# Kernel optimization log

Measured on AMD Instinct MI355X. Metric: run time of the kernel, lower is better.

The kernel has to match this reference:

```python
import jax, jax.numpy as jnp
import numpy as np

N, E, G = 50000, 800000, 1024
F_IN, GH, HEADS, MH = 128, 64, 4, 64
C1 = GH // 2  # 32 per-head channels in gat1


def _p(key, shape, scale=0.05):
    return (scale * jax.random.normal(key, shape)).astype(jnp.float32)


def setup_inputs() -> dict:
    key = jax.random.key(0)
    ks = jax.random.split(key, 24)
    x = jax.random.normal(ks[0], (N, F_IN), dtype=jnp.float32)
    edge_index = jax.random.randint(ks[1], (2, E), 0, N, dtype=jnp.int64)
    batch = jnp.sort(jax.random.randint(ks[2], (N,), 0, G, dtype=jnp.int64))
    return {
        "x": x, "edge_index": edge_index, "batch": batch,
        # node_proj
        "Wp": _p(ks[3], (F_IN, GH)), "bp": jnp.zeros((GH,), jnp.float32),
        # gat1: in GH, out C1 per head, 4 heads, concat
        "W1": _p(ks[4], (GH, HEADS * C1)), "as1": _p(ks[5], (HEADS, C1)),
        "ad1": _p(ks[6], (HEADS, C1)), "b1": jnp.zeros((HEADS * C1,), jnp.float32),
        # gat2: in HEADS*C1=128, out GH, 1 head, no concat
        "W2": _p(ks[7], (HEADS * C1, GH)), "as2": _p(ks[8], (1, GH)),
        "ad2": _p(ks[9], (1, GH)), "b2": jnp.zeros((GH,), jnp.float32),
        # mlp + heads
        "Wm1": _p(ks[10], (GH, MH)), "bm1": jnp.zeros((MH,), jnp.float32),
        "Wm2": _p(ks[11], (MH, MH)), "bm2": jnp.zeros((MH,), jnp.float32),
        "Wc": _p(ks[12], (MH, 1)), "bc": jnp.zeros((1,), jnp.float32),
        "Wr": _p(ks[13], (MH, 1)), "br": jnp.zeros((1,), jnp.float32),
        "Wv": _p(ks[14], (MH, 1)), "bv": jnp.zeros((1,), jnp.float32),
    }


def gat_conv(h, src, dst, W, att_src, att_dst, bias, heads, out_ch, concat):
    n = h.shape[0]
    xh = (h @ W).reshape(n, heads, out_ch)          # [N,H,C]
    a_s = jnp.einsum("nhc,hc->nh", xh, att_src)      # [N,H]
    a_d = jnp.einsum("nhc,hc->nh", xh, att_dst)
    e = jax.nn.leaky_relu(a_s[src] + a_d[dst], 0.2)  # [E,H]
    # segment softmax over incoming edges of each dst node
    m = jax.ops.segment_max(e, dst, num_segments=n)
    e = jnp.exp(e - m[dst])
    denom = jax.ops.segment_sum(e, dst, num_segments=n)
    alpha = e / (denom[dst] + 1e-16)                 # [E,H]
    msg = xh[src] * alpha[:, :, None]                # [E,H,C]
    out = jax.ops.segment_sum(msg, dst, num_segments=n)
    out = out.reshape(n, heads * out_ch) if concat else out.mean(axis=1)
    return out + bias


def reference(x, edge_index, batch, Wp, bp, W1, as1, ad1, b1, W2, as2, ad2, b2,
              Wm1, bm1, Wm2, bm2, Wc, bc, Wr, br, Wv, bv):
    n = x.shape[0]
    loops = jnp.arange(n, dtype=edge_index.dtype)
    src = jnp.concatenate([edge_index[0], loops])  # PyG add_self_loops=True
    dst = jnp.concatenate([edge_index[1], loops])

    h = jax.nn.relu(x @ Wp + bp)
    h = jax.nn.elu(gat_conv(h, src, dst, W1, as1, ad1, b1, HEADS, C1, True))
    h = jax.nn.elu(gat_conv(h, src, dst, W2, as2, ad2, b2, 1, GH, False))

    # global mean pool over graphs
    sums = jax.ops.segment_sum(h, batch, num_segments=G)
    cnts = jax.ops.segment_sum(jnp.ones((n,), h.dtype), batch, num_segments=G)
    hg = sums / jnp.maximum(cnts, 1.0)[:, None]      # [G, GH]

    z = jax.nn.relu(hg @ Wm1 + bm1)
    z = jax.nn.relu(z @ Wm2 + bm2)
    class_logit = (z @ Wc + bc)[:, 0]
    ret = (z @ Wr + br)[:, 0]
    vol = jax.nn.softplus((z @ Wv + bv)[:, 0])
    return class_logit, ret, vol
```

## Files before the change

kernel.cpp:

```cpp
#include <hip/hip_runtime.h>
#include <hip/hip_bf16.h>
#include <math.h>

#define F_IN 128
#define GH   64

typedef __attribute__((ext_vector_type(8))) short bf16x8;
typedef __attribute__((ext_vector_type(4))) float f32x4;

__device__ __forceinline__ void edge_sd(const int* __restrict__ ei, int E, int e, int& s, int& d) {
    if (e < E) { s = ei[e]; d = ei[E + e]; } else { s = d = e - E; }
}
__device__ __forceinline__ float leaky(float x) { return (x >= 0.f) ? x : 0.2f * x; }
__device__ __forceinline__ unsigned short f2bf(float f) {
    unsigned u = __float_as_uint(f);
    u += 0x7FFFu + ((u >> 16) & 1u);
    return (unsigned short)(u >> 16);
}
__device__ __forceinline__ float bflo(unsigned v) { return __uint_as_float(v << 16); }
__device__ __forceinline__ float bfhi(unsigned v) { return __uint_as_float(v & 0xFFFF0000u); }

template<int K, int M, bool RELU, int AIN, int DOTS>
__global__ __launch_bounds__(256) void gemm_mfma(
    const float* __restrict__ Xf, const unsigned short* __restrict__ Xb,
    const float* __restrict__ W, const float* __restrict__ Bias,
    unsigned short* __restrict__ Yb,
    const float* __restrict__ asw, const float* __restrict__ adw,
    float* __restrict__ as_n, float* __restrict__ ad_n, int nrows)
{
    constexpr int KP = K + 8;
    __shared__ unsigned short Als[64 * KP];
    __shared__ unsigned short Wls[M * KP];
    const int t = threadIdx.x;
    const int base = blockIdx.x * 64;

    for (int i = t; i < K * M / 4; i += 256) {
        int k  = i / (M / 4);
        int m0 = (i % (M / 4)) * 4;
        float4 wv = ((const float4*)W)[i];
        Wls[(m0 + 0) * KP + k] = f2bf(wv.x);
        Wls[(m0 + 1) * KP + k] = f2bf(wv.y);
        Wls[(m0 + 2) * KP + k] = f2bf(wv.z);
        Wls[(m0 + 3) * KP + k] = f2bf(wv.w);
    }
    if (AIN == 0) {
        for (int i = t; i < 64 * K / 4; i += 256) {
            int r  = i / (K / 4);
            int c4 = (i % (K / 4)) * 4;
            int n = base + r;
            float4 v = make_float4(0.f, 0.f, 0.f, 0.f);
            if (n < nrows) v = ((const float4*)(Xf + (size_t)n * K))[c4 >> 2];
            ushort4 pk = make_ushort4(f2bf(v.x), f2bf(v.y), f2bf(v.z), f2bf(v.w));
            *(ushort4*)&Als[r * KP + c4] = pk;
        }
    } else {
        for (int i = t; i < 64 * K / 8; i += 256) {
            int r  = i / (K / 8);
            int c8 = (i % (K / 8)) * 8;
            int n = base + r;
            uint4 v = make_uint4(0, 0, 0, 0);
            if (n < nrows) v = ((const uint4*)(Xb + (size_t)n * K))[c8 >> 3];
            *(uint4*)&Als[r * KP + c8] = v;
        }
    }
    __syncthreads();

    const int w = t >> 6, l = t & 63;
    const int lr = l & 15, lg = l >> 4;
    constexpr int CT = M / 16;
    f32x4 acc[CT];
#pragma unroll
    for (int ct = 0; ct < CT; ct++) acc[ct] = (f32x4){0.f, 0.f, 0.f, 0.f};

    const unsigned short* arow = &Als[(w * 16 + lr) * KP + lg * 8];
#pragma unroll
    for (int ks = 0; ks < K / 32; ks++) {
        bf16x8 a = *(const bf16x8*)(arow + ks * 32);
#pragma unroll
        for (int ct = 0; ct < CT; ct++) {
            bf16x8 b = *(const bf16x8*)&Wls[(ct * 16 + lr) * KP + ks * 32 + lg * 8];
            acc[ct] = __builtin_amdgcn_mfma_f32_16x16x32_bf16(a, b, acc[ct], 0, 0, 0);
        }
    }

#pragma unroll
    for (int ct = 0; ct < CT; ct++) {
        int col = ct * 16 + lr;
        float bb = Bias ? Bias[col] : 0.f;
#pragma unroll
        for (int r = 0; r < 4; r++) {
            int gr = base + w * 16 + lg * 4 + r;
            if (gr < nrows) {
                float v = acc[ct][r] + bb;
                if (RELU) v = fmaxf(v, 0.f);
                Yb[(size_t)gr * M + col] = f2bf(v);
            }
        }
    }

    if (DOTS == 1) {
        float hs[4][4], hd[4][4];
#pragma unroll
        for (int r = 0; r < 4; r++)
#pragma unroll
            for (int h = 0; h < 4; h++) { hs[r][h] = 0.f; hd[r][h] = 0.f; }
#pragma unroll
        for (int ct = 0; ct < CT; ct++) {
            int col = ct * 16 + lr;
            float aw = asw[col], dw = adw[col];
            int h = ct >> 1;
#pragma unroll
            for (int r = 0; r < 4; r++) {
                hs[r][h] += acc[ct][r] * aw;
                hd[r][h] += acc[ct][r] * dw;
            }
        }
#pragma unroll
        for (int msk = 8; msk >= 1; msk >>= 1) {
#pragma unroll
            for (int r = 0; r < 4; r++)
#pragma unroll
                for (int h = 0; h < 4; h++) {
                    hs[r][h] += __shfl_xor(hs[r][h], msk);
                    hd[r][h] += __shfl_xor(hd[r][h], msk);
                }
        }
        if (lr == 0) {
#pragma unroll
            for (int r = 0; r < 4; r++) {
                int gr = base + w * 16 + lg * 4 + r;
                if (gr < nrows) {
                    ((float4*)as_n)[gr] = make_float4(hs[r][0], hs[r][1], hs[r][2], hs[r][3]);
                    ((float4*)ad_n)[gr] = make_float4(hd[r][0], hd[r][1], hd[r][2], hd[r][3]);
                }
            }
        }
    } else if (DOTS == 2) {
        float ps[4], pd[4];
#pragma unroll
        for (int r = 0; r < 4; r++) { ps[r] = 0.f; pd[r] = 0.f; }
#pragma unroll
        for (int ct = 0; ct < CT; ct++) {
            int col = ct * 16 + lr;
            float aw = asw[col], dw = adw[col];
#pragma unroll
            for (int r = 0; r < 4; r++) {
                ps[r] += acc[ct][r] * aw;
                pd[r] += acc[ct][r] * dw;
            }
        }
#pragma unroll
        for (int msk = 8; msk >= 1; msk >>= 1) {
#pragma unroll
            for (int r = 0; r < 4; r++) {
                ps[r] += __shfl_xor(ps[r], msk);
                pd[r] += __shfl_xor(pd[r], msk);
            }
        }
        if (lr == 0) {
#pragma unroll
            for (int r = 0; r < 4; r++) {
                int gr = base + w * 16 + lg * 4 + r;
                if (gr < nrows) { as_n[gr] = ps[r]; ad_n[gr] = pd[r]; }
            }
        }
    }
}

__global__ __launch_bounds__(256) void bucket_hist(
    const int* __restrict__ ei, int E, int ET, int N, int* __restrict__ bcnt)
{
    __shared__ int h[256];
    h[threadIdx.x] = 0;
    __syncthreads();
    for (int e = blockIdx.x * 256 + threadIdx.x; e < ET; e += gridDim.x * 256) {
        int s, d; edge_sd(ei, E, e, s, d);
        if ((unsigned)s < (unsigned)N && (unsigned)d < (unsigned)N)
            atomicAdd(&h[d >> 8], 1);
    }
    __syncthreads();
    if (h[threadIdx.x]) atomicAdd(&bcnt[threadIdx.x], h[threadIdx.x]);
}

__global__ __launch_bounds__(256) void bucket_scan(
    const int* __restrict__ bcnt, int* __restrict__ bbase, int* __restrict__ bcur,
    int* __restrict__ row_start, int B, int N)
{
    __shared__ int wsum[4];
    int t = threadIdx.x, lane = t & 63, w = t >> 6;
    int v = (t < B) ? bcnt[t] : 0;
    int incl = v;
#pragma unroll
    for (int off = 1; off < 64; off <<= 1) {
        int n = __shfl_up(incl, off);
        if (lane >= off) incl += n;
    }
    if (lane == 63) wsum[w] = incl;
    __syncthreads();
    int wb = 0;
#pragma unroll
    for (int i = 0; i < 4; i++) if (i < w) wb += wsum[i];
    int excl = wb + incl - v;
    if (t < B) { bbase[t] = excl; bcur[t] = excl; }
    if (t == 255) { bbase[B] = excl + v; row_start[N] = excl + v; }
}

#define SCHUNK 4096
__global__ __launch_bounds__(256) void bucket_scatter(
    const int* __restrict__ ei, int E, int ET, int N,
    int* __restrict__ bcur, int* __restrict__ deg, uint2* __restrict__ staged)
{
    __shared__ int bc[256];
    __shared__ int bb[256];
    const int t = threadIdx.x;
    const int base = blockIdx.x * SCHUNK;
    bc[t] = 0;
    __syncthreads();
    const int cnt = min(SCHUNK, ET - base);
    int ss[16], dd[16], lr[16];
#pragma unroll
    for (int k = 0; k < 16; k++) {
        int i = t + k * 256;
        ss[k] = -1; dd[k] = 0; lr[k] = 0;
        if (i < cnt) {
            int s, d; edge_sd(ei, E, base + i, s, d);
            if ((unsigned)s < (unsigned)N && (unsigned)d < (unsigned)N) {
                ss[k] = s; dd[k] = d;
                lr[k] = atomicAdd(&bc[d >> 8], 1);
                atomicAdd(&deg[d], 1);
            }
        }
    }
    __syncthreads();
    bb[t] = bc[t] ? atomicAdd(&bcur[t], bc[t]) : 0;
    __syncthreads();
#pragma unroll
    for (int k = 0; k < 16; k++) {
        if (ss[k] >= 0)
            staged[bb[dd[k] >> 8] + lr[k]] = make_uint2((unsigned)ss[k], (unsigned)dd[k]);
    }
}

__global__ __launch_bounds__(256) void row_scan(
    const int* __restrict__ deg, const int* __restrict__ bbase,
    int* __restrict__ row_start, int N)
{
    __shared__ int wsum[4];
    const int b = blockIdx.x, t = threadIdx.x;
    const int lane = t & 63, w = t >> 6;
    const int node = b * 256 + t;
    int v = (node < N) ? deg[node] : 0;
    int incl = v;
#pragma unroll
    for (int off = 1; off < 64; off <<= 1) {
        int n = __shfl_up(incl, off);
        if (lane >= off) incl += n;
    }
    if (lane == 63) wsum[w] = incl;
    __syncthreads();
    int wb = 0;
#pragma unroll
    for (int i = 0; i < 4; i++) if (i < w) wb += wsum[i];
    if (node < N) row_start[node] = bbase[b] + wb + incl - v;
}

__global__ __launch_bounds__(256) void bucket_final(
    const uint2* __restrict__ staged, const int* __restrict__ bbase,
    const int* __restrict__ row_start, int* __restrict__ adj, int N)
{
    __shared__ int cur[256];
    const int b = blockIdx.x, t = threadIdx.x;
    const int node = b * 256 + t;
    cur[t] = (node < N) ? row_start[node] : 0;
    __syncthreads();
    const int beg = bbase[b], end = bbase[b + 1];
    for (int i = beg + t; i < end; i += 256) {
        uint2 sd = staged[i];
        int pos = atomicAdd(&cur[sd.y & 255], 1);
        adj[pos] = (int)sd.x;
    }
}

__global__ __launch_bounds__(256) void gat1_fused(
    const int* __restrict__ row_start, const int* __restrict__ adj,
    const float* __restrict__ as_n, const float* __restrict__ ad_n,
    const unsigned short* __restrict__ xhb, const float* __restrict__ b1,
    unsigned short* __restrict__ outb, int N)
{
    __shared__ unsigned s_ofs[4][64];
    __shared__ float    s_p[4][256];
    const int w = threadIdx.x >> 6;
    const int d = blockIdx.x * 4 + w;
    if (d >= N) return;
    const int lane = threadIdx.x & 63;
    const int li = lane & 31;
    const int half = lane >> 5;
    const int h = li >> 3;
    const int beg = row_start[d];
    const int deg = row_start[d + 1] - beg;
    const float4 adv = ((const float4*)ad_n)[d];
    const char* xbase = (const char*)xhb;

    float l0 = 0.f, l1 = 0.f, l2 = 0.f, l3 = 0.f;
    float a0 = 0.f, a1 = 0.f, a2 = 0.f, a3 = 0.f;
    for (int j0 = 0; j0 < deg; j0 += 64) {
        const int chunk = min(64, deg - j0);
        if (lane < chunk) {
            int s = adj[beg + j0 + lane];
            float4 asv = ((const float4*)as_n)[s];
            float p0 = __expf(leaky(asv.x + adv.x));
            float p1 = __expf(leaky(asv.y + adv.y));
            float p2 = __expf(leaky(asv.z + adv.z));
            float p3 = __expf(leaky(asv.w + adv.w));
            l0 += p0; l1 += p1; l2 += p2; l3 += p3;
            s_ofs[w][lane] = (unsigned)s << 8;
            ((float4*)&s_p[w][lane * 4])[0] = make_float4(p0, p1, p2, p3);
        }
        __threadfence_block();
#pragma unroll 4
        for (int jj = half; jj < chunk; jj += 2) {
            float a = s_p[w][jj * 4 + h];
            unsigned ofs = s_ofs[w][jj] + ((unsigned)li << 3);
            uint2 u = *(const uint2*)(xbase + ofs);
            a0 += a * bflo(u.x); a1 += a * bfhi(u.x);
            a2 += a * bflo(u.y); a3 += a * bfhi(u.y);
        }
        __threadfence_block();
    }
    a0 += __shfl_xor(a0, 32); a1 += __shfl_xor(a1, 32);
    a2 += __shfl_xor(a2, 32); a3 += __shfl_xor(a3, 32);
#pragma unroll
    for (int msk = 32; msk >= 1; msk >>= 1) {
        l0 += __shfl_xor(l0, msk); l1 += __shfl_xor(l1, msk);
        l2 += __shfl_xor(l2, msk); l3 += __shfl_xor(l3, msk);
    }
    if (half == 0) {
        float lh = (h == 0) ? l0 : (h == 1) ? l1 : (h == 2) ? l2 : l3;
        const float inv = 1.0f / (lh + 1e-16f);
        float4 bb = ((const float4*)b1)[li];
        float v0 = a0 * inv + bb.x;
        float v1 = a1 * inv + bb.y;
        float v2 = a2 * inv + bb.z;
        float v3 = a3 * inv + bb.w;
        v0 = (v0 > 0.f) ? v0 : expm1f(v0);
        v1 = (v1 > 0.f) ? v1 : expm1f(v1);
        v2 = (v2 > 0.f) ? v2 : expm1f(v2);
        v3 = (v3 > 0.f) ? v3 : expm1f(v3);
        unsigned pk01 = (unsigned)f2bf(v0) | ((unsigned)f2bf(v1) << 16);
        unsigned pk23 = (unsigned)f2bf(v2) | ((unsigned)f2bf(v3) << 16);
        ((uint2*)((char*)outb + (size_t)d * 256))[li] = make_uint2(pk01, pk23);
    }
}

__global__ __launch_bounds__(256) void gat2_fused(
    const int* __restrict__ row_start, const int* __restrict__ adj,
    const float* __restrict__ as_n, const float* __restrict__ ad_n,
    const unsigned short* __restrict__ xhb, const float* __restrict__ b2,
    const int* __restrict__ batch, float* __restrict__ sums, float* __restrict__ cnts,
    int N, int G)
{
    __shared__ unsigned s_ofs[4][64];
    __shared__ float    s_p[4][64];
    __shared__ float    pbuf[4][64];
    __shared__ int      pg[4];
    const int w = threadIdx.x >> 6;
    const int d = blockIdx.x * 4 + w;
    const int lane = threadIdx.x & 63;
    const int li = lane & 31;
    const int half = lane >> 5;
    const bool alive = (d < N);
    int beg = 0, deg = 0; float ad = 0.f; int g = -1;
    if (alive) {
        beg = row_start[d];
        deg = row_start[d + 1] - beg;
        ad = ad_n[d];
        int gb = batch[d];
        if ((unsigned)gb < (unsigned)G) g = gb;
    }
    const char* xbase = (const char*)xhb;
    float l = 0.f, a0 = 0.f, a1 = 0.f;
    for (int j0 = 0; j0 < deg; j0 += 64) {
        const int chunk = min(64, deg - j0);
        if (lane < chunk) {
            int s = adj[beg + j0 + lane];
            float p = __expf(leaky(as_n[s] + ad));
            l += p;
            s_ofs[w][lane] = (unsigned)s << 7;
            s_p[w][lane] = p;
        }
        __threadfence_block();
#pragma unroll 4
        for (int jj = half; jj < chunk; jj += 2) {
            float a = s_p[w][jj];
            unsigned ofs = s_ofs[w][jj] + ((unsigned)li << 2);
            unsigned u = *(const unsigned*)(xbase + ofs);
            a0 += a * bflo(u);
            a1 += a * bfhi(u);
        }
        __threadfence_block();
    }
    a0 += __shfl_xor(a0, 32);
    a1 += __shfl_xor(a1, 32);
#pragma unroll
    for (int msk = 32; msk >= 1; msk >>= 1) l += __shfl_xor(l, msk);

    if (lane == 0) pg[w] = g;
    if (half == 0) {
        const float inv = 1.0f / (l + 1e-16f);
        float2 bb = ((const float2*)b2)[li];
        float v0 = a0 * inv + bb.x;
        float v1 = a1 * inv + bb.y;
        v0 = (v0 > 0.f) ? v0 : expm1f(v0);
        v1 = (v1 > 0.f) ? v1 : expm1f(v1);
        ((float2*)&pbuf[w][2 * li])[0] = make_float2((g >= 0) ? v0 : 0.f,
                                                    (g >= 0) ? v1 : 0.f);
    }
    __syncthreads();
    int g0 = pg[0], g1 = pg[1], g2 = pg[2], g3 = pg[3];
    bool uni = (g0 >= 0) && (g1 == g0) && (g2 == g0) && (g3 == g0);
    if (uni) {
        if (w == 0) {
            float s4 = pbuf[0][lane] + pbuf[1][lane] + pbuf[2][lane] + pbuf[3][lane];
            atomicAdd(&sums[(size_t)g0 * 64 + lane], s4);
            if (lane == 0) atomicAdd(&cnts[g0], 4.0f);
        }
    } else if (g >= 0) {
        atomicAdd(&sums[(size_t)g * 64 + lane], pbuf[w][lane]);
        if (lane == 0) atomicAdd(&cnts[g], 1.0f);
    }
}

__global__ __launch_bounds__(64) void mlp_head(
    const float* __restrict__ sums, const float* __restrict__ cnts,
    const float* __restrict__ Wm1, const float* __restrict__ bm1,
    const float* __restrict__ Wm2, const float* __restrict__ bm2,
    const float* __restrict__ Wc, const float* __restrict__ bc,
    const float* __restrict__ Wr, const float* __restrict__ br,
    const float* __restrict__ Wv, const float* __restrict__ bv,
    float* __restrict__ out, int G)
{
    int g = blockIdx.x;
    int t = threadIdx.x;
    __shared__ float hrow[64];
    __shared__ float zrow[64];
    float hv = sums[(size_t)g * 64 + t] / fmaxf(cnts[g], 1.0f);
    hrow[t] = hv;
    __syncthreads();
    float z1 = bm1[t];
#pragma unroll 8
    for (int k = 0; k < 64; k++) z1 += hrow[k] * Wm1[k * 64 + t];
    z1 = fmaxf(z1, 0.f);
    zrow[t] = z1;
    __syncthreads();
    float z2 = bm2[t];
#pragma unroll 8
    for (int k = 0; k < 64; k++) z2 += zrow[k] * Wm2[k * 64 + t];
    z2 = fmaxf(z2, 0.f);
    float pc = z2 * Wc[t], pr = z2 * Wr[t], pv = z2 * Wv[t];
#pragma unroll
    for (int m = 32; m >= 1; m >>= 1) {
        pc += __shfl_xor(pc, m);
        pr += __shfl_xor(pr, m);
        pv += __shfl_xor(pv, m);
    }
    if (t == 0) {
        out[g] = pc + bc[0];
        out[G + g] = pr + br[0];
        float s = pv + bv[0];
        out[2 * G + g] = (s > 20.f) ? s : log1pf(expf(s));
    }
}

extern "C" void kernel_launch(void* const* d_in, const int* in_sizes, int n_in,
                              void* d_out, int out_size, void* d_ws, size_t ws_size,
                              hipStream_t stream)
{
    const float* x     = (const float*)d_in[0];
    const int*   ei    = (const int*)d_in[1];
    const int*   batch = (const int*)d_in[2];
    const float* Wp  = (const float*)d_in[3];
    const float* bp  = (const float*)d_in[4];
    const float* W1  = (const float*)d_in[5];
    const float* as1 = (const float*)d_in[6];
    const float* ad1 = (const float*)d_in[7];
    const float* b1  = (const float*)d_in[8];
    const float* W2  = (const float*)d_in[9];
    const float* as2 = (const float*)d_in[10];
    const float* ad2 = (const float*)d_in[11];
    const float* b2  = (const float*)d_in[12];
    const float* Wm1 = (const float*)d_in[13];
    const float* bm1 = (const float*)d_in[14];
    const float* Wm2 = (const float*)d_in[15];
    const float* bm2 = (const float*)d_in[16];
    const float* Wc  = (const float*)d_in[17];
    const float* bc  = (const float*)d_in[18];
    const float* Wr  = (const float*)d_in[19];
    const float* br  = (const float*)d_in[20];
    const float* Wv  = (const float*)d_in[21];
    const float* bv  = (const float*)d_in[22];

    const int N  = in_sizes[0] / F_IN;
    const int E  = in_sizes[1] / 2;
    const int G  = out_size / 3;
    const int ET = E + N;
    const int B  = (N + 255) >> 8;

    float* ws = (float*)d_ws;
    size_t o = 0;
    unsigned short* h0b  = (unsigned short*)(ws + o); o += (size_t)N * 32;
    unsigned short* h1b  = (unsigned short*)(ws + o); o += (size_t)N * 64;
    unsigned short* xhb1 = (unsigned short*)(ws + o); o += (size_t)N * 64;
    unsigned short* xhb2 = (unsigned short*)(ws + o); o += (size_t)N * 32;
    float* as1n = ws + o; o += (size_t)N * 4;
    float* ad1n = ws + o; o += (size_t)N * 4;
    float* as2n = ws + o; o += (size_t)N;
    float* ad2n = ws + o; o += (size_t)N;
    int* row_start = (int*)(ws + o); o += (size_t)N + 1;
    int* adj       = (int*)(ws + o); o += (size_t)ET;
    int* bbase     = (int*)(ws + o); o += 257;
    int* bcur      = (int*)(ws + o); o += 256;
    uint2* staged  = (uint2*)(ws + o); o += (size_t)ET * 2;
    float* zstart = ws + o;
    int*   deg  = (int*)(ws + o); o += (size_t)N;
    int*   bcnt = (int*)(ws + o); o += 256;
    float* sums = ws + o;         o += (size_t)G * 64;
    float* cnts = ws + o;         o += (size_t)G;
    size_t zlen = (size_t)(ws + o - zstart) * sizeof(float);

    hipMemsetAsync(zstart, 0, zlen, stream);

    const int gN64 = (N + 63) / 64;
    const int gN4  = (N + 3) / 4;
    const int gSC  = (ET + SCHUNK - 1) / SCHUNK;

    bucket_hist<<<512, 256, 0, stream>>>(ei, E, ET, N, bcnt);
    bucket_scan<<<1, 256, 0, stream>>>(bcnt, bbase, bcur, row_start, B, N);
    bucket_scatter<<<gSC, 256, 0, stream>>>(ei, E, ET, N, bcur, deg, staged);
    row_scan<<<B, 256, 0, stream>>>(deg, bbase, row_start, N);
    bucket_final<<<B, 256, 0, stream>>>(staged, bbase, row_start, adj, N);

    gemm_mfma<128, 64, true, 0, 0><<<gN64, 256, 0, stream>>>(
        x, nullptr, Wp, bp, h0b, nullptr, nullptr, nullptr, nullptr, N);
    gemm_mfma<64, 128, false, 1, 1><<<gN64, 256, 0, stream>>>(
        nullptr, h0b, W1, nullptr, xhb1, as1, ad1, as1n, ad1n, N);
    gat1_fused<<<gN4, 256, 0, stream>>>(row_start, adj, as1n, ad1n, xhb1, b1, h1b, N);
    gemm_mfma<128, 64, false, 1, 2><<<gN64, 256, 0, stream>>>(
        nullptr, h1b, W2, nullptr, xhb2, as2, ad2, as2n, ad2n, N);
    gat2_fused<<<gN4, 256, 0, stream>>>(row_start, adj, as2n, ad2n, xhb2, b2,
                                        batch, sums, cnts, N, G);
    mlp_head<<<G, 64, 0, stream>>>(sums, cnts, Wm1, bm1, Wm2, bm2,
                                   Wc, bc, Wr, br, Wv, bv, (float*)d_out, G);
}
```

Measured before the change: 321.2 us.

## Locally sort edges in LDS and pack staged entries to cut CSR build traffic

The bucket scatter now counts per-bucket edges in shared memory, sorts each chunk's edges by bucket in LDS, and writes them to the staging buffer as contiguous runs. Each edge is packed into one 32-bit word (bucket, low dst bits, src), replacing the 8-byte pair. The global per-node degree atomics and the separate row_scan kernel are gone: a new bucket_build kernel counts degrees per bucket in LDS, scans them to write row_start, and fills adj. This aims to remove global atomic contention, scattered staging writes and one launch, at the cost of reading the edge list twice and limiting node ids to 16 bits (N < 65536).

After: 293.6 us. 8.6% less time.

```diff
diff --git a/kernel.cpp b/kernel.cpp
--- a/kernel.cpp
+++ b/kernel.cpp
@@ -205,79 +205,99 @@
     if (t == 255) { bbase[B] = excl + v; row_start[N] = excl + v; }
 }
 
-#define SCHUNK 4096
+#define SCHUNK 2048
 __global__ __launch_bounds__(256) void bucket_scatter(
     const int* __restrict__ ei, int E, int ET, int N,
-    int* __restrict__ bcur, int* __restrict__ deg, uint2* __restrict__ staged)
+    int* __restrict__ bcur, unsigned* __restrict__ staged)
 {
     __shared__ int bc[256];
+    __shared__ int lbase[256];
     __shared__ int bb[256];
+    __shared__ unsigned sorted[SCHUNK];
+    __shared__ int wsum[4];
     const int t = threadIdx.x;
+    const int lane = t & 63, wv = t >> 6;
     const int base = blockIdx.x * SCHUNK;
+    const int cnt = min(SCHUNK, ET - base);
     bc[t] = 0;
     __syncthreads();
-    const int cnt = min(SCHUNK, ET - base);
-    int ss[16], dd[16], lr[16];
-#pragma unroll
-    for (int k = 0; k < 16; k++) {
-        int i = t + k * 256;
-        ss[k] = -1; dd[k] = 0; lr[k] = 0;
-        if (i < cnt) {
-            int s, d; edge_sd(ei, E, base + i, s, d);
-            if ((unsigned)s < (unsigned)N && (unsigned)d < (unsigned)N) {
-                ss[k] = s; dd[k] = d;
-                lr[k] = atomicAdd(&bc[d >> 8], 1);
-                atomicAdd(&deg[d], 1);
-            }
-        }
-    }
-    __syncthreads();
-    bb[t] = bc[t] ? atomicAdd(&bcur[t], bc[t]) : 0;
-    __syncthreads();
-#pragma unroll
-    for (int k = 0; k < 16; k++) {
-        if (ss[k] >= 0)
-            staged[bb[dd[k] >> 8] + lr[k]] = make_uint2((unsigned)ss[k], (unsigned)dd[k]);
-    }
-}
-
-__global__ __launch_bounds__(256) void row_scan(
-    const int* __restrict__ deg, const int* __restrict__ bbase,
-    int* __restrict__ row_start, int N)
-{
-    __shared__ int wsum[4];
-    const int b = blockIdx.x, t = threadIdx.x;
-    const int lane = t & 63, w = t >> 6;
-    const int node = b * 256 + t;
-    int v = (node < N) ? deg[node] : 0;
+    for (int i = t; i < cnt; i += 256) {
+        int s, d; edge_sd(ei, E, base + i, s, d);
+        if ((unsigned)s < (unsigned)N && (unsigned)d < (unsigned)N)
+            atomicAdd(&bc[d >> 8], 1);
+    }
+    __syncthreads();
+    int v = bc[t];
     int incl = v;
 #pragma unroll
     for (int off = 1; off < 64; off <<= 1) {
         int n = __shfl_up(incl, off);
         if (lane >= off) incl += n;
     }
-    if (lane == 63) wsum[w] = incl;
+    if (lane == 63) wsum[wv] = incl;
     __syncthreads();
     int wb = 0;
 #pragma unroll
-    for (int i = 0; i < 4; i++) if (i < w) wb += wsum[i];
-    if (node < N) row_start[node] = bbase[b] + wb + incl - v;
-}
-
-__global__ __launch_bounds__(256) void bucket_final(
-    const uint2* __restrict__ staged, const int* __restrict__ bbase,
-    const int* __restrict__ row_start, int* __restrict__ adj, int N)
-{
-    __shared__ int cur[256];
+    for (int i = 0; i < 4; i++) if (i < wv) wb += wsum[i];
+    int excl = wb + incl - v;
+    lbase[t] = excl;
+    bb[t] = v ? atomicAdd(&bcur[t], v) : 0;
+    __syncthreads();
+    bc[t] = excl;
+    __syncthreads();
+    for (int i = t; i < cnt; i += 256) {
+        int s, d; edge_sd(ei, E, base + i, s, d);
+        if ((unsigned)s < (unsigned)N && (unsigned)d < (unsigned)N) {
+            int b = d >> 8;
+            int r = atomicAdd(&bc[b], 1);
+            sorted[r] = ((unsigned)b << 24) | ((unsigned)(d & 255) << 16) | (unsigned)s;
+        }
+    }
+    __syncthreads();
+    const int total = bc[255];
+    for (int i = t; i < total; i += 256) {
+        unsigned wd = sorted[i];
+        int b = wd >> 24;
+        staged[bb[b] + (i - lbase[b])] = wd;
+    }
+}
+
+__global__ __launch_bounds__(256) void bucket_build(
+    const unsigned* __restrict__ staged, const int* __restrict__ bbase,
+    int* __restrict__ row_start, int* __restrict__ adj, int N)
+{
+    __shared__ int cnt2[256];
+    __shared__ int cur2[256];
+    __shared__ int wsum[4];
     const int b = blockIdx.x, t = threadIdx.x;
-    const int node = b * 256 + t;
-    cur[t] = (node < N) ? row_start[node] : 0;
-    __syncthreads();
+    const int lane = t & 63, wv = t >> 6;
     const int beg = bbase[b], end = bbase[b + 1];
+    cnt2[t] = 0;
+    __syncthreads();
+    for (int i = beg + t; i < end; i += 256)
+        atomicAdd(&cnt2[(staged[i] >> 16) & 255], 1);
+    __syncthreads();
+    int v = cnt2[t];
+    int incl = v;
+#pragma unroll
+    for (int off = 1; off < 64; off <<= 1) {
+        int n = __shfl_up(incl, off);
+        if (lane >= off) incl += n;
+    }
+    if (lane == 63) wsum[wv] = incl;
+    __syncthreads();
+    int wb = 0;
+#pragma unroll
+    for (int i = 0; i < 4; i++) if (i < wv) wb += wsum[i];
+    int excl = beg + wb + incl - v;
+    int node = b * 256 + t;
+    if (node < N) row_start[node] = excl;
+    cur2[t] = excl;
+    __syncthreads();
     for (int i = beg + t; i < end; i += 256) {
-        uint2 sd = staged[i];
-        int pos = atomicAdd(&cur[sd.y & 255], 1);
-        adj[pos] = (int)sd.x;
+        unsigned wd = staged[i];
+        int pos = atomicAdd(&cur2[(wd >> 16) & 255], 1);
+        adj[pos] = (int)(wd & 0xFFFFu);
     }
 }
 
@@ -519,9 +539,8 @@
     int* adj       = (int*)(ws + o); o += (size_t)ET;
     int* bbase     = (int*)(ws + o); o += 257;
     int* bcur      = (int*)(ws + o); o += 256;
-    uint2* staged  = (uint2*)(ws + o); o += (size_t)ET * 2;
+    unsigned* staged = (unsigned*)(ws + o); o += (size_t)ET;
     float* zstart = ws + o;
-    int*   deg  = (int*)(ws + o); o += (size_t)N;
     int*   bcnt = (int*)(ws + o); o += 256;
     float* sums = ws + o;         o += (size_t)G * 64;
     float* cnts = ws + o;         o += (size_t)G;
@@ -535,9 +554,8 @@
 
     bucket_hist<<<512, 256, 0, stream>>>(ei, E, ET, N, bcnt);
     bucket_scan<<<1, 256, 0, stream>>>(bcnt, bbase, bcur, row_start, B, N);
-    bucket_scatter<<<gSC, 256, 0, stream>>>(ei, E, ET, N, bcur, deg, staged);
-    row_scan<<<B, 256, 0, stream>>>(deg, bbase, row_start, N);
-    bucket_final<<<B, 256, 0, stream>>>(staged, bbase, row_start, adj, N);
+    bucket_scatter<<<gSC, 256, 0, stream>>>(ei, E, ET, N, bcur, staged);
+    bucket_build<<<B, 256, 0, stream>>>(staged, bbase, row_start, adj, N);
 
     gemm_mfma<128, 64, true, 0, 0><<<gN64, 256, 0, stream>>>(
         x, nullptr, Wp, bp, h0b, nullptr, nullptr, nullptr, nullptr, N);
```
